# Kernel tuning notes

Hardware: AMD Instinct MI355X
Metric: run time of the kernel (lower is better)

## Reference

```python
import jax, jax.numpy as jnp
import numpy as np

L = 37       # num_landmarks
K = 8        # neighbors per landmark (uniform stand-in for ragged heatmap_dict)
HM = 512     # full heatmap size
HS = 128     # heatmap_size * scale_factor_heatmap (0.25)
HC = 64      # heatmap_size * scale_factor_cond (0.125)
DELTA = 1e-6
SP_BETA = 5.0
FFT_N = 384  # >= 255 + 128 - 1 = 382 (linear-conv safe FFT size)
BN_EPS = 1e-5


def softplus_b(x):
    # torch nn.Softplus(beta=5): log(1 + exp(beta*x)) / beta
    return jax.nn.softplus(SP_BETA * x) / SP_BETA


def resize_cubic(x, h, w):
    # stands in for F.interpolate(mode='bicubic', align_corners=False)
    return jax.image.resize(x, x.shape[:-2] + (h, w), method='cubic')


def setup_inputs() -> dict:
    key = jax.random.key(0)
    k1, k2, k3 = jax.random.split(key, 3)
    heatmaps = jax.random.normal(k1, (2, L, HM, HM), dtype=jnp.float32)
    cond_heatmaps = jax.random.normal(k2, (L, K, HC, HC), dtype=jnp.float32)
    bias = jax.random.uniform(k3, (L, K, HS, HS), dtype=jnp.float32) * 0.01
    bn_gamma = jnp.ones((L,), dtype=jnp.float32)
    bn_beta = jnp.zeros((L,), dtype=jnp.float32)
    valid_idx = jnp.asarray(
        np.stack([[(i + 1 + k) % L for k in range(K)] for i in range(L)]),
        dtype=jnp.int32)
    return {"heatmaps": heatmaps, "cond_heatmaps": cond_heatmaps, "bias": bias,
            "bn_gamma": bn_gamma, "bn_beta": bn_beta, "valid_idx": valid_idx}


def reference(heatmaps, cond_heatmaps, bias, bn_gamma, bn_beta, valid_idx):
    B = heatmaps.shape[0]
    # BatchNorm2d in training mode (batch statistics, biased variance)
    mean = jnp.mean(heatmaps, axis=(0, 2, 3))
    var = jnp.var(heatmaps, axis=(0, 2, 3))
    scale = (bn_gamma / jnp.sqrt(var + BN_EPS))[None, :, None, None]
    hm = (heatmaps - mean[None, :, None, None]) * scale + bn_beta[None, :, None, None]

    # downsample heatmaps to 128x128
    hm_rs = resize_cubic(hm, HS, HS)                      # [B, L, 128, 128]

    # priors: 64 -> 128 upsample, then softplus. [L, K, 128, 128]
    prior = softplus_b(resize_cubic(cond_heatmaps, HS, HS))

    # likelihoods: gather conditioning channels. [B, L, K, 128, 128]
    like = softplus_b(hm_rs[:, valid_idx])

    # conv_fft: pad (63, 64) each spatial side -> 255; flipped-kernel fft_conv
    # == true linear convolution, valid output 255-128+1 = 128
    pad = (HS - 1) // 2
    like_p = jnp.pad(like, ((0, 0), (0, 0), (0, 0), (pad, pad + 1), (pad, pad + 1)))
    Fb = jnp.fft.rfft2(like_p, s=(FFT_N, FFT_N))
    Fa = jnp.fft.rfft2(prior, s=(FFT_N, FFT_N))
    conv = jnp.fft.irfft2(Fb * Fa[None], s=(FFT_N, FFT_N))
    conv = conv[..., HS - 1:2 * HS - 1, HS - 1:2 * HS - 1]  # [B, L, K, 128, 128]

    # log-sum over conditioning landmarks, with learnable bias
    energy = jnp.sum(jnp.log(conv + softplus_b(bias)[None] + DELTA), axis=2)  # [B, L, 128, 128]

    # upsample x4 back to 512 and add initial (local) log-energy
    energy = resize_cubic(energy, HM, HM) + jnp.log(softplus_b(hm) + DELTA)

    # differentiable argmax2d (temperature = 1), meshgrid indexing='ij':
    # xx varies along dim -2, yy along dim -1 (as in the original code)
    soft = jax.nn.softmax(energy.reshape(B, L, -1), axis=-1).reshape(B, L, HM, HM)
    xx = jnp.arange(HM, dtype=energy.dtype)[:, None]
    yy = jnp.arange(HM, dtype=energy.dtype)[None, :]
    ex = jnp.sum(soft * xx, axis=(-2, -1))
    ey = jnp.sum(soft * yy, axis=(-2, -1))
    ones = jnp.ones_like(ex)
    return jnp.stack([ones, ex, ey], axis=-1)  # [B, L, 3]
```

## Files before the change

kernel.cpp:

```cpp
#include <hip/hip_runtime.h>
#include <hip/hip_bf16.h>
#include <math.h>

#define L_ 37
#define K_ 8
#define HM_ 512
#define HS_ 128
#define HC_ 64

using f32x4 = __attribute__((ext_vector_type(4))) float;

#define L_REGION 24656
#define PB_OFF   L_REGION
#define CONV_LDS (PB_OFF + 158*128)

static constexpr size_t OFF_SUMS   = 0;
static constexpr size_t OFF_PARAMS = 512;
static constexpr size_t OFF_TAJ    = 1024;
static constexpr size_t OFF_TAW    = 1536;
static constexpr size_t OFF_TBJ    = 9728;
static constexpr size_t OFF_TBW    = 10240;
static constexpr size_t OFF_TCJ    = 12288;
static constexpr size_t OFF_TCW    = 14336;
static constexpr size_t OFF_PART   = 22528;
static constexpr size_t OFF_TMPA   = 32768;
static constexpr size_t OFF_HMRS   = OFF_TMPA + (size_t)74*128*512*4;
static constexpr size_t OFF_PIMG   = OFF_HMRS + (size_t)74*16384*4;
static constexpr size_t OFF_EALL   = OFF_PIMG + (size_t)296*16384;
static constexpr size_t OFF_E128   = OFF_EALL + (size_t)592*16384*4;

__device__ __forceinline__ float keys_cubic(float x) {
  float out = ((1.5f * x - 2.5f) * x) * x + 1.f;
  if (x >= 1.f) out = ((-0.5f * x + 2.5f) * x - 4.f) * x + 2.f;
  if (x >= 2.f) out = 0.f;
  return out;
}
__device__ __forceinline__ float sp(float x) {
  float z = 5.f * x;
  return (fmaxf(z, 0.f) + log1pf(expf(-fabsf(z)))) * 0.2f;
}

__global__ void bn_partial_k(const float* __restrict__ heat, float* __restrict__ sums) {
  int l = blockIdx.x >> 4, seg = blockIdx.x & 15;
  int tid = threadIdx.x;
  float s = 0.f, q = 0.f;
  for (int i = tid; i < 8192; i += 256) {
    int f4 = seg * 8192 + i;
    int b = f4 >> 16, rem = f4 & 65535;
    float4 v = ((const float4*)heat)[(size_t)(b * L_ + l) * 65536 + rem];
    s += v.x + v.y + v.z + v.w;
    q += v.x*v.x + v.y*v.y + v.z*v.z + v.w*v.w;
  }
  __shared__ float rs[256], rq[256];
  rs[tid] = s; rq[tid] = q; __syncthreads();
  for (int o = 128; o > 0; o >>= 1) {
    if (tid < o) { rs[tid] += rs[tid + o]; rq[tid] += rq[tid + o]; }
    __syncthreads();
  }
  if (tid == 0) { atomicAdd(&sums[2*l], rs[0]); atomicAdd(&sums[2*l+1], rq[0]); }
}

__global__ void tables_k(int* taj, float* taw, int* tbj, float* tbw, int* tcj, float* tcw,
                         const float* __restrict__ sums, const float* __restrict__ gamma,
                         const float* __restrict__ beta, float* __restrict__ params) {
  int i = threadIdx.x;
  if (i < 128) {
    float sf = 4.f * i + 1.5f;
    int j0 = 4 * i - 6;
    taj[i] = j0;
    float w[16], sum = 0.f;
    for (int t = 0; t < 16; ++t) {
      int j = j0 + t; float ww = 0.f;
      if (j >= 0 && j < 512) ww = keys_cubic(fabsf(sf - (float)j) * 0.25f);
      w[t] = ww; sum += ww;
    }
    for (int t = 0; t < 16; ++t) taw[i*16 + t] = w[t] / sum;
    float sb = 0.5f * i - 0.25f;
    int jb = (int)floorf(sb) - 1;
    tbj[i] = jb;
    float wb[4], sumb = 0.f;
    for (int t = 0; t < 4; ++t) {
      int j = jb + t; float ww = 0.f;
      if (j >= 0 && j < 64) ww = keys_cubic(fabsf(sb - (float)j));
      wb[t] = ww; sumb += ww;
    }
    for (int t = 0; t < 4; ++t) tbw[i*4 + t] = wb[t] / sumb;
  }
  if (i < 512) {
    float sc = 0.25f * i - 0.375f;
    int jc = (int)floorf(sc) - 1;
    tcj[i] = jc;
    float wc[4], sumc = 0.f;
    for (int t = 0; t < 4; ++t) {
      int j = jc + t; float ww = 0.f;
      if (j >= 0 && j < 128) ww = keys_cubic(fabsf(sc - (float)j));
      wc[t] = ww; sumc += ww;
    }
    for (int t = 0; t < 4; ++t) tcw[i*4 + t] = wc[t] / sumc;
  }
  if (i < L_) {
    float inv = 1.f / (2.f * HM_ * HM_);
    float mean = sums[2*i] * inv;
    float var  = sums[2*i+1] * inv - mean * mean;
    float sc = gamma[i] * rsqrtf(var + 1e-5f);
    params[2*i] = sc;
    params[2*i+1] = beta[i] - mean * sc;
  }
}

__global__ void down_rows_k(const float* __restrict__ heat, const float* __restrict__ params,
                            const int* __restrict__ taj, const float* __restrict__ taw,
                            float* __restrict__ tmpA) {
  int bl = blockIdx.x >> 7;
  int i  = blockIdx.x & 127;
  int l = bl % L_;
  float sc = params[2*l], sh = params[2*l+1];
  int j0 = taj[i];
  const float* base = heat + (size_t)bl * (HM_*HM_);
  float* out = tmpA + ((size_t)bl * 128 + i) * HM_;
  float w[16];
  #pragma unroll
  for (int t = 0; t < 16; ++t) w[t] = taw[i*16 + t];
  for (int c = threadIdx.x; c < HM_; c += 256) {
    float acc = 0.f;
    #pragma unroll
    for (int t = 0; t < 16; ++t) {
      int j = min(511, max(0, j0 + t));
      acc = fmaf(w[t], fmaf(base[(size_t)j*HM_ + c], sc, sh), acc);
    }
    out[c] = acc;
  }
}

__global__ void down_cols_k(const float* __restrict__ tmpA, const int* __restrict__ taj,
                            const float* __restrict__ taw, float* __restrict__ hmrs) {
  __shared__ float row[HM_];
  int bl = blockIdx.x >> 7, i = blockIdx.x & 127;
  const float* src = tmpA + ((size_t)bl * 128 + i) * HM_;
  for (int c = threadIdx.x; c < HM_; c += 128) row[c] = src[c];
  __syncthreads();
  int ic = threadIdx.x;
  int j0 = taj[ic];
  float acc = 0.f;
  #pragma unroll
  for (int t = 0; t < 16; ++t) {
    int j = min(511, max(0, j0 + t));
    acc = fmaf(taw[ic*16 + t], row[j], acc);
  }
  hmrs[((size_t)bl * 128 + i) * 128 + ic] = acc;
}

__global__ void prior_rev_k(const float* __restrict__ cond, const int* __restrict__ tbj,
                            const float* __restrict__ tbw, unsigned char* __restrict__ pimg) {
  __shared__ float c64[HC_*HC_];
  int lk = blockIdx.x;
  const float* src = cond + (size_t)lk * HC_*HC_;
  for (int i = threadIdx.x; i < HC_*HC_; i += 256) c64[i] = src[i];
  __syncthreads();
  for (int t = threadIdx.x; t < 2048; t += 256) {
    int s = t >> 4, jblk = t & 15;
    int jy0 = tbj[s];
    float wy[4]; int jys[4];
    #pragma unroll
    for (int q = 0; q < 4; ++q) { wy[q] = tbw[s*4+q]; jys[q] = min(63, max(0, jy0 + q)); }
    float v[8];
    #pragma unroll
    for (int ii = 0; ii < 8; ++ii) {
      int j = jblk * 8 + ii;
      int jx0 = tbj[j];
      float acc = 0.f;
      #pragma unroll
      for (int q = 0; q < 4; ++q) {
        int jy = jys[q];
        float r = 0.f;
        #pragma unroll
        for (int tx = 0; tx < 4; ++tx) {
          int jx = min(63, max(0, jx0 + tx));
          r = fmaf(tbw[j*4 + tx], c64[jy*64 + jx], r);
        }
        acc = fmaf(wy[q], r, acc);
      }
      v[ii] = sp(acc);
    }
    int w0 = 0, w1 = 0;
    w0 = __builtin_amdgcn_cvt_pk_fp8_f32(v[7], v[6], w0, false);
    w0 = __builtin_amdgcn_cvt_pk_fp8_f32(v[5], v[4], w0, true);
    w1 = __builtin_amdgcn_cvt_pk_fp8_f32(v[3], v[2], w1, false);
    w1 = __builtin_amdgcn_cvt_pk_fp8_f32(v[1], v[0], w1, true);
    int cc = (15 - jblk) ^ (s & 7);
    uint2* dst = (uint2*)(pimg + (size_t)lk * 16384 + s * 128 + cc * 8);
    *dst = make_uint2((unsigned)w0, (unsigned)w1);
  }
}

__global__ __launch_bounds__(512) void conv_mfma_k(
    const float* __restrict__ hmrs, const unsigned char* __restrict__ pimg,
    const float* __restrict__ bias, const int* __restrict__ vidx,
    float* __restrict__ e_all) {
  extern __shared__ char lds[];
  int blk = blockIdx.x;
  int b = blk / 296, lk = blk % 296;
  int tid = threadIdx.x;

  {
    unsigned* lz = (unsigned*)lds;
    for (int i = tid; i < 16 + 4 + 2048; i += 512) {
      int a;
      if (i < 16) a = i;
      else if (i < 20) a = 6160 + (i - 16);
      else { int g = i - 20; int u = g >> 4, c = g & 15; a = 48*u + 48 + c; }
      lz[a] = 0u;
    }
  }
  {
    unsigned* pz = (unsigned*)(lds + PB_OFF);
    for (int i = tid; i < 960; i += 512) {
      int a = (i < 480) ? i : (18304/4 + (i - 480));
      pz[a] = 0u;
    }
  }
  int vl = vidx[lk];
  const float4* likes4 = (const float4*)(hmrs + (size_t)(b * L_ + vl) * 16384);
  for (int i = tid; i < 1024; i += 512) {
    int u = i >> 3, c16 = (i & 7) << 4;
    int base4 = u * 32 + (c16 >> 2);
    unsigned wds[4];
    #pragma unroll
    for (int q = 0; q < 4; ++q) {
      float4 v = likes4[base4 + q];
      int w = 0;
      w = __builtin_amdgcn_cvt_pk_fp8_f32(sp(v.x), sp(v.y), w, false);
      w = __builtin_amdgcn_cvt_pk_fp8_f32(sp(v.z), sp(v.w), w, true);
      wds[q] = (unsigned)w;
    }
    *(uint4*)(lds + 64 + 192*u + c16) = make_uint4(wds[0], wds[1], wds[2], wds[3]);
  }
  {
    const uint4* src = (const uint4*)(pimg + (size_t)lk * 16384);
    uint4* dst = (uint4*)(lds + PB_OFF + 15*128);
    for (int i = tid; i < 1024; i += 512) dst[i] = src[i];
  }
  __syncthreads();

  int wid = tid >> 6, lane = tid & 63;
  int wm = wid >> 2, wn = wid & 3;
  int l15 = lane & 15, kg = lane >> 4;
  int xb = wn * 32;
  int par4 = (1 + l15) & 3;
  int shiftB = par4 << 3;
  int C0 = 1 + l15 + 8*kg + xb - par4;

  f32x4 acc[4][2];
  #pragma unroll
  for (int mt = 0; mt < 4; ++mt)
    #pragma unroll
    for (int nt = 0; nt < 2; ++nt)
      #pragma unroll
      for (int j = 0; j < 4; ++j) acc[mt][nt][j] = 0.f;

  int u_lo = max(0, 64 * wm - 63);
  for (int u = u_lo; u <= 127; ++u) {
    const unsigned* bp = (const unsigned*)(lds + C0 + 192*u);
    #pragma unroll
    for (int kc = 0; kc < 4; ++kc) {
      if (xb + 95 - 32*kc < 0 || xb + 33 - 32*kc > 127) continue;
      long Bf[2];
      #pragma unroll
      for (int nt = 0; nt < 2; ++nt) {
        int q = 24 + 4*nt - 8*kc;
        unsigned d0 = bp[q], d1 = bp[q+1], d2 = bp[q+2];
        unsigned b0 = (unsigned)((((unsigned long long)d1 << 32) | d0) >> shiftB);
        unsigned b1 = (unsigned)((((unsigned long long)d2 << 32) | d1) >> shiftB);
        Bf[nt] = (long)(((unsigned long long)b1 << 32) | b0);
      }
      int cA16 = (12 - 4*kc + kg);
      #pragma unroll
      for (int mt = 0; mt < 4; ++mt) {
        int y0 = 64 * wm + 16 * mt;
        if (u < y0 - 63 || u > y0 + 79) continue;
        int rr = y0 + l15 + 79 - u;
        int swz = (cA16 ^ ((rr + 1) & 7)) << 3;
        long Af = *(const long*)(lds + PB_OFF + rr * 128 + swz);
        acc[mt][0] = __builtin_amdgcn_mfma_f32_16x16x32_fp8_fp8(Af, Bf[0], acc[mt][0], 0, 0, 0);
        acc[mt][1] = __builtin_amdgcn_mfma_f32_16x16x32_fp8_fp8(Af, Bf[1], acc[mt][1], 0, 0, 0);
      }
    }
  }

  const float* bs = bias + (size_t)lk * 16384;
  float* eo = e_all + (size_t)(b * 296 + lk) * 16384;
  int row0 = kg * 4;
  #pragma unroll
  for (int mt = 0; mt < 4; ++mt) {
    #pragma unroll
    for (int nt = 0; nt < 2; ++nt) {
      int x = xb + nt * 16 + l15;
      int yb = 64 * wm + 16 * mt + row0;
      #pragma unroll
      for (int rr = 0; rr < 4; ++rr) {
        int y = yb + rr;
        float v = acc[mt][nt][rr] + sp(bs[y * 128 + x]) + 1e-6f;
        eo[y * 128 + x] = logf(v);
      }
    }
  }
}

__global__ void esum_k(const float* __restrict__ e_all, float* __restrict__ e128) {
  int bl = blockIdx.x; int tid = threadIdx.x;
  const float4* src = (const float4*)(e_all + (size_t)bl * 8 * 16384);
  float4* dst = (float4*)(e128 + (size_t)bl * 16384);
  for (int i = tid; i < 4096; i += 256) {
    float4 a = src[i];
    #pragma unroll
    for (int k = 1; k < 8; ++k) {
      float4 v = src[k * 4096 + i];
      a.x += v.x; a.y += v.y; a.z += v.z; a.w += v.w;
    }
    dst[i] = a;
  }
}

__global__ __launch_bounds__(256) void final_partial_k(
    const float* __restrict__ heat, const float* __restrict__ params,
    const float* __restrict__ e128, const int* __restrict__ tcj, const float* __restrict__ tcw,
    float* __restrict__ partials) {
  __shared__ float Elds[20 * 128];
  __shared__ float rm[256], rS[256], ry[256], rx[256];
  int blk = blockIdx.x;
  int bl = blk >> 3, seg = blk & 7;
  int l = bl % L_;
  int tid = threadIdx.x;
  float sc = params[2*l], sh = params[2*l+1];
  int y_lo = seg * 64;
  int r_lo = max(0, tcj[y_lo]);
  int r_hi = min(127, tcj[y_lo + 63] + 3);
  int nrows = r_hi - r_lo + 1;
  const float* E = e128 + (size_t)bl * 16384;
  for (int i = tid; i < nrows * 128; i += 256) Elds[i] = E[r_lo * 128 + i];
  __syncthreads();

  float wx[2][4]; int jx[2][4];
  #pragma unroll
  for (int xi = 0; xi < 2; ++xi) {
    int x = tid + xi * 256;
    int j0 = tcj[x];
    #pragma unroll
    for (int t = 0; t < 4; ++t) { wx[xi][t] = tcw[x*4 + t]; jx[xi][t] = min(127, max(0, j0 + t)); }
  }

  float m = -1e30f, S = 0.f, Sy = 0.f, Sx = 0.f;
  for (int y = y_lo; y < y_lo + 64; ++y) {
    int jy0 = tcj[y];
    float wy[4]; int jyr[4];
    #pragma unroll
    for (int t = 0; t < 4; ++t) { wy[t] = tcw[y*4 + t]; jyr[t] = min(127, max(0, jy0 + t)) - r_lo; }
    #pragma unroll
    for (int xi = 0; xi < 2; ++xi) {
      int x = tid + xi * 256;
      float a = 0.f;
      #pragma unroll
      for (int t = 0; t < 4; ++t) {
        const float* Er = Elds + jyr[t] * 128;
        float rrow = wx[xi][0]*Er[jx[xi][0]] + wx[xi][1]*Er[jx[xi][1]]
                   + wx[xi][2]*Er[jx[xi][2]] + wx[xi][3]*Er[jx[xi][3]];
        a = fmaf(wy[t], rrow, a);
      }
      float hm = fmaf(heat[(size_t)bl * 262144 + y * 512 + x], sc, sh);
      float e = a + logf(sp(hm) + 1e-6f);
      if (e > m) {
        float f = expf(m - e);
        S *= f; Sy *= f; Sx *= f; m = e;
      }
      float w = expf(e - m);
      S += w; Sy = fmaf(w, (float)y, Sy); Sx = fmaf(w, (float)x, Sx);
    }
  }
  rm[tid] = m; rS[tid] = S; ry[tid] = Sy; rx[tid] = Sx; __syncthreads();
  for (int o = 128; o > 0; o >>= 1) {
    if (tid < o) {
      float ma = rm[tid], mb = rm[tid + o];
      float M = fmaxf(ma, mb);
      float fa = expf(ma - M), fb = expf(mb - M);
      rS[tid] = rS[tid]*fa + rS[tid+o]*fb;
      ry[tid] = ry[tid]*fa + ry[tid+o]*fb;
      rx[tid] = rx[tid]*fa + rx[tid+o]*fb;
      rm[tid] = M;
    }
    __syncthreads();
  }
  if (tid == 0) {
    float* p = partials + (size_t)blk * 4;
    p[0] = rm[0]; p[1] = rS[0]; p[2] = ry[0]; p[3] = rx[0];
  }
}

__global__ void final_combine_k(const float* __restrict__ partials, float* __restrict__ out) {
  int bl = blockIdx.x;
  if (threadIdx.x != 0) return;
  float M = -1e30f, S = 0.f, Sy = 0.f, Sx = 0.f;
  for (int i = 0; i < 8; ++i) {
    const float* p = partials + (size_t)(bl * 8 + i) * 4;
    float m2 = p[0], s2 = p[1], sy2 = p[2], sx2 = p[3];
    float Mn = fmaxf(M, m2);
    float fa = expf(M - Mn), fb = expf(m2 - Mn);
    S = S*fa + s2*fb; Sy = Sy*fa + sy2*fb; Sx = Sx*fa + sx2*fb; M = Mn;
  }
  out[bl*3 + 0] = 1.f;
  out[bl*3 + 1] = Sy / S;
  out[bl*3 + 2] = Sx / S;
}

extern "C" void kernel_launch(void* const* d_in, const int* in_sizes, int n_in,
                              void* d_out, int out_size, void* d_ws, size_t ws_size,
                              hipStream_t stream) {
  const float* heat  = (const float*)d_in[0];
  const float* cond  = (const float*)d_in[1];
  const float* bias  = (const float*)d_in[2];
  const float* gamma = (const float*)d_in[3];
  const float* beta  = (const float*)d_in[4];
  const int*   vidx  = (const int*)d_in[5];
  float* out = (float*)d_out;
  char* ws = (char*)d_ws;

  float* sums   = (float*)(ws + OFF_SUMS);
  float* params = (float*)(ws + OFF_PARAMS);
  int*   taj = (int*)(ws + OFF_TAJ);   float* taw = (float*)(ws + OFF_TAW);
  int*   tbj = (int*)(ws + OFF_TBJ);   float* tbw = (float*)(ws + OFF_TBW);
  int*   tcj = (int*)(ws + OFF_TCJ);   float* tcw = (float*)(ws + OFF_TCW);
  float* part  = (float*)(ws + OFF_PART);
  float* tmpA  = (float*)(ws + OFF_TMPA);
  float* hmrs  = (float*)(ws + OFF_HMRS);
  unsigned char* pimg = (unsigned char*)(ws + OFF_PIMG);
  float* e_all = (float*)(ws + OFF_EALL);
  float* e128  = (float*)(ws + OFF_E128);

  hipFuncSetAttribute((const void*)conv_mfma_k,
                      hipFuncAttributeMaxDynamicSharedMemorySize, CONV_LDS);

  hipMemsetAsync(sums, 0, 2 * L_ * sizeof(float), stream);
  bn_partial_k<<<L_ * 16, 256, 0, stream>>>(heat, sums);
  tables_k<<<1, 512, 0, stream>>>(taj, taw, tbj, tbw, tcj, tcw, sums, gamma, beta, params);
  down_rows_k<<<74 * 128, 256, 0, stream>>>(heat, params, taj, taw, tmpA);
  down_cols_k<<<74 * 128, 128, 0, stream>>>(tmpA, taj, taw, hmrs);
  prior_rev_k<<<L_ * K_, 256, 0, stream>>>(cond, tbj, tbw, pimg);
  conv_mfma_k<<<2 * L_ * K_, 512, CONV_LDS, stream>>>(hmrs, pimg, bias, vidx, e_all);
  esum_k<<<74, 256, 0, stream>>>(e_all, e128);
  final_partial_k<<<74 * 8, 256, 0, stream>>>(heat, params, e128, tcj, tcw, part);
  final_combine_k<<<74, 64, 0, stream>>>(part, out);
}
```

Baseline: 657.0 us.

## Fuse downsample passes, switch conv to scaled MFMA, atomically reduce energies

Measured after the change: 979.6 us. 1.49x slower.

```diff
diff --git a/kernel.cpp b/kernel.cpp
--- a/kernel.cpp
+++ b/kernel.cpp
@@ -9,10 +9,10 @@
 #define HC_ 64
 
 using f32x4 = __attribute__((ext_vector_type(4))) float;
-
-#define L_REGION 24656
-#define PB_OFF   L_REGION
-#define CONV_LDS (PB_OFF + 158*128)
+typedef int i32x8 __attribute__((ext_vector_type(8)));
+
+#define PB_OFF   32768
+#define CONV_LDS (PB_OFF + 160*128)
 
 static constexpr size_t OFF_SUMS   = 0;
 static constexpr size_t OFF_PARAMS = 512;
@@ -23,11 +23,9 @@
 static constexpr size_t OFF_TCJ    = 12288;
 static constexpr size_t OFF_TCW    = 14336;
 static constexpr size_t OFF_PART   = 22528;
-static constexpr size_t OFF_TMPA   = 32768;
-static constexpr size_t OFF_HMRS   = OFF_TMPA + (size_t)74*128*512*4;
+static constexpr size_t OFF_HMRS   = 32768;
 static constexpr size_t OFF_PIMG   = OFF_HMRS + (size_t)74*16384*4;
-static constexpr size_t OFF_EALL   = OFF_PIMG + (size_t)296*16384;
-static constexpr size_t OFF_E128   = OFF_EALL + (size_t)592*16384*4;
+static constexpr size_t OFF_E128   = OFF_PIMG + (size_t)296*16384;
 
 __device__ __forceinline__ float keys_cubic(float x) {
   float out = ((1.5f * x - 2.5f) * x) * x + 1.f;
@@ -108,46 +106,43 @@
   }
 }
 
-__global__ void down_rows_k(const float* __restrict__ heat, const float* __restrict__ params,
-                            const int* __restrict__ taj, const float* __restrict__ taw,
-                            float* __restrict__ tmpA) {
-  int bl = blockIdx.x >> 7;
-  int i  = blockIdx.x & 127;
-  int l = bl % L_;
-  float sc = params[2*l], sh = params[2*l+1];
-  int j0 = taj[i];
-  const float* base = heat + (size_t)bl * (HM_*HM_);
-  float* out = tmpA + ((size_t)bl * 128 + i) * HM_;
-  float w[16];
-  #pragma unroll
-  for (int t = 0; t < 16; ++t) w[t] = taw[i*16 + t];
-  for (int c = threadIdx.x; c < HM_; c += 256) {
-    float acc = 0.f;
+__global__ __launch_bounds__(256) void down_fused_k(
+    const float* __restrict__ heat, const int* __restrict__ taj,
+    const float* __restrict__ taw, float* __restrict__ hmrs) {
+  extern __shared__ float sds[];
+  float* in = sds;
+  float* rm = sds + 28*512;
+  int bl = blockIdx.x >> 5, ig = blockIdx.x & 31;
+  int i0 = ig * 4;
+  int j00 = 4*i0 - 6;
+  int tid = threadIdx.x;
+  const float* hb = heat + (size_t)bl * 262144;
+  for (int idx = tid; idx < 28*128; idx += 256) {
+    int jr = idx >> 7, c4 = (idx & 127) << 2;
+    int j = min(511, max(0, j00 + jr));
+    *(float4*)(in + jr*512 + c4) = *(const float4*)(hb + (size_t)j*512 + c4);
+  }
+  __syncthreads();
+  for (int idx = tid; idx < 2048; idx += 256) {
+    int ri = idx >> 9, c = idx & 511;
+    const float* wt = taw + (i0 + ri) * 16;
+    float a = 0.f;
+    #pragma unroll
+    for (int t = 0; t < 16; ++t) a = fmaf(wt[t], in[(4*ri + t)*512 + c], a);
+    rm[ri*512 + c] = a;
+  }
+  __syncthreads();
+  for (int idx = tid; idx < 512; idx += 256) {
+    int ri = idx >> 7, ic = idx & 127;
+    int j0 = taj[ic];
+    float a = 0.f;
     #pragma unroll
     for (int t = 0; t < 16; ++t) {
       int j = min(511, max(0, j0 + t));
-      acc = fmaf(w[t], fmaf(base[(size_t)j*HM_ + c], sc, sh), acc);
-    }
-    out[c] = acc;
-  }
-}
-
-__global__ void down_cols_k(const float* __restrict__ tmpA, const int* __restrict__ taj,
-                            const float* __restrict__ taw, float* __restrict__ hmrs) {
-  __shared__ float row[HM_];
-  int bl = blockIdx.x >> 7, i = blockIdx.x & 127;
-  const float* src = tmpA + ((size_t)bl * 128 + i) * HM_;
-  for (int c = threadIdx.x; c < HM_; c += 128) row[c] = src[c];
-  __syncthreads();
-  int ic = threadIdx.x;
-  int j0 = taj[ic];
-  float acc = 0.f;
-  #pragma unroll
-  for (int t = 0; t < 16; ++t) {
-    int j = min(511, max(0, j0 + t));
-    acc = fmaf(taw[ic*16 + t], row[j], acc);
-  }
-  hmrs[((size_t)bl * 128 + i) * 128 + ic] = acc;
+      a = fmaf(taw[ic*16 + t], rm[ri*512 + j], a);
+    }
+    hmrs[((size_t)bl*128 + i0 + ri)*128 + ic] = a;
+  }
 }
 
 __global__ void prior_rev_k(const float* __restrict__ cond, const int* __restrict__ tbj,
@@ -157,168 +152,156 @@
   const float* src = cond + (size_t)lk * HC_*HC_;
   for (int i = threadIdx.x; i < HC_*HC_; i += 256) c64[i] = src[i];
   __syncthreads();
-  for (int t = threadIdx.x; t < 2048; t += 256) {
-    int s = t >> 4, jblk = t & 15;
+  for (int t = threadIdx.x; t < 1024; t += 256) {
+    int s = t >> 3, c16 = t & 7;
     int jy0 = tbj[s];
     float wy[4]; int jys[4];
     #pragma unroll
     for (int q = 0; q < 4; ++q) { wy[q] = tbw[s*4+q]; jys[q] = min(63, max(0, jy0 + q)); }
-    float v[8];
-    #pragma unroll
-    for (int ii = 0; ii < 8; ++ii) {
-      int j = jblk * 8 + ii;
-      int jx0 = tbj[j];
-      float acc = 0.f;
+    unsigned w[4];
+    #pragma unroll
+    for (int q = 0; q < 4; ++q) {
+      float vv[4];
       #pragma unroll
-      for (int q = 0; q < 4; ++q) {
-        int jy = jys[q];
-        float r = 0.f;
+      for (int bq = 0; bq < 4; ++bq) {
+        int jj = 16*c16 + 4*q + bq;
+        int j = 127 - jj;
+        int jx0 = tbj[j];
+        float acc = 0.f;
         #pragma unroll
-        for (int tx = 0; tx < 4; ++tx) {
-          int jx = min(63, max(0, jx0 + tx));
-          r = fmaf(tbw[j*4 + tx], c64[jy*64 + jx], r);
+        for (int ty = 0; ty < 4; ++ty) {
+          float r = 0.f;
+          #pragma unroll
+          for (int tx = 0; tx < 4; ++tx) {
+            int jx = min(63, max(0, jx0 + tx));
+            r = fmaf(tbw[j*4 + tx], c64[jys[ty]*64 + jx], r);
+          }
+          acc = fmaf(wy[ty], r, acc);
         }
-        acc = fmaf(wy[q], r, acc);
+        vv[bq] = sp(acc);
       }
-      v[ii] = sp(acc);
-    }
-    int w0 = 0, w1 = 0;
-    w0 = __builtin_amdgcn_cvt_pk_fp8_f32(v[7], v[6], w0, false);
-    w0 = __builtin_amdgcn_cvt_pk_fp8_f32(v[5], v[4], w0, true);
-    w1 = __builtin_amdgcn_cvt_pk_fp8_f32(v[3], v[2], w1, false);
-    w1 = __builtin_amdgcn_cvt_pk_fp8_f32(v[1], v[0], w1, true);
-    int cc = (15 - jblk) ^ (s & 7);
-    uint2* dst = (uint2*)(pimg + (size_t)lk * 16384 + s * 128 + cc * 8);
-    *dst = make_uint2((unsigned)w0, (unsigned)w1);
-  }
-}
-
-__global__ __launch_bounds__(512) void conv_mfma_k(
+      int wq = 0;
+      wq = __builtin_amdgcn_cvt_pk_fp8_f32(vv[0], vv[1], wq, false);
+      wq = __builtin_amdgcn_cvt_pk_fp8_f32(vv[2], vv[3], wq, true);
+      w[q] = (unsigned)wq;
+    }
+    unsigned char* dst = pimg + (size_t)lk*16384 + s*128 + ((c16 ^ (s & 7)) << 4);
+    *(uint4*)dst = make_uint4(w[0], w[1], w[2], w[3]);
+  }
+}
+
+__global__ __launch_bounds__(256, 3) void conv_mfma_k(
     const float* __restrict__ hmrs, const unsigned char* __restrict__ pimg,
     const float* __restrict__ bias, const int* __restrict__ vidx,
-    float* __restrict__ e_all) {
+    const float* __restrict__ params, float* __restrict__ e128) {
   extern __shared__ char lds[];
+  char* Lb = lds;
+  char* Pb = lds + PB_OFF;
   int blk = blockIdx.x;
-  int b = blk / 296, lk = blk % 296;
+  int b = blk / 296, lk = blk % 296, l = lk >> 3;
   int tid = threadIdx.x;
 
   {
-    unsigned* lz = (unsigned*)lds;
-    for (int i = tid; i < 16 + 4 + 2048; i += 512) {
-      int a;
-      if (i < 16) a = i;
-      else if (i < 20) a = 6160 + (i - 16);
-      else { int g = i - 20; int u = g >> 4, c = g & 15; a = 48*u + 48 + c; }
-      lz[a] = 0u;
+    unsigned* lz = (unsigned*)Lb;
+    for (int i = tid; i < 4096; i += 256) {
+      int row = i >> 5, q = i & 31;
+      lz[row*64 + (q < 16 ? q : q + 32)] = 0u;
     }
   }
   {
-    unsigned* pz = (unsigned*)(lds + PB_OFF);
-    for (int i = tid; i < 960; i += 512) {
-      int a = (i < 480) ? i : (18304/4 + (i - 480));
-      pz[a] = 0u;
+    unsigned* pz = (unsigned*)Pb;
+    for (int i = tid; i < 1024; i += 256) {
+      int row = i >> 5;
+      pz[(row < 16 ? row : row + 128)*32 + (i & 31)] = 0u;
     }
   }
   int vl = vidx[lk];
+  float sc = params[2*vl], sh = params[2*vl + 1];
   const float4* likes4 = (const float4*)(hmrs + (size_t)(b * L_ + vl) * 16384);
-  for (int i = tid; i < 1024; i += 512) {
-    int u = i >> 3, c16 = (i & 7) << 4;
-    int base4 = u * 32 + (c16 >> 2);
+  for (int i = tid; i < 1024; i += 256) {
+    int u = i >> 3, ch = i & 7;
+    int b4 = u * 32 + ch * 4;
     unsigned wds[4];
     #pragma unroll
     for (int q = 0; q < 4; ++q) {
-      float4 v = likes4[base4 + q];
+      float4 v = likes4[b4 + q];
       int w = 0;
-      w = __builtin_amdgcn_cvt_pk_fp8_f32(sp(v.x), sp(v.y), w, false);
-      w = __builtin_amdgcn_cvt_pk_fp8_f32(sp(v.z), sp(v.w), w, true);
+      w = __builtin_amdgcn_cvt_pk_fp8_f32(sp(fmaf(v.x, sc, sh)), sp(fmaf(v.y, sc, sh)), w, false);
+      w = __builtin_amdgcn_cvt_pk_fp8_f32(sp(fmaf(v.z, sc, sh)), sp(fmaf(v.w, sc, sh)), w, true);
       wds[q] = (unsigned)w;
     }
-    *(uint4*)(lds + 64 + 192*u + c16) = make_uint4(wds[0], wds[1], wds[2], wds[3]);
+    *(uint4*)(Lb + u*256 + 64 + ch*16) = make_uint4(wds[0], wds[1], wds[2], wds[3]);
   }
   {
     const uint4* src = (const uint4*)(pimg + (size_t)lk * 16384);
-    uint4* dst = (uint4*)(lds + PB_OFF + 15*128);
-    for (int i = tid; i < 1024; i += 512) dst[i] = src[i];
+    uint4* dst = (uint4*)(Pb + 16*128);
+    for (int i = tid; i < 1024; i += 256) dst[i] = src[i];
   }
   __syncthreads();
 
   int wid = tid >> 6, lane = tid & 63;
-  int wm = wid >> 2, wn = wid & 3;
+  int wm = wid >> 1, wn = wid & 1;
   int l15 = lane & 15, kg = lane >> 4;
-  int xb = wn * 32;
-  int par4 = (1 + l15) & 3;
-  int shiftB = par4 << 3;
-  int C0 = 1 + l15 + 8*kg + xb - par4;
-
-  f32x4 acc[4][2];
+  int x0 = wn * 64, y_base = wm * 64;
+  int bb = 1 + x0 + l15 + 32*kg;
+  int bd0 = bb >> 2;
+  int shiftB = (bb & 3) * 8;
+
+  f32x4 acc[4][4];
   #pragma unroll
   for (int mt = 0; mt < 4; ++mt)
     #pragma unroll
-    for (int nt = 0; nt < 2; ++nt)
+    for (int nt = 0; nt < 4; ++nt)
       #pragma unroll
       for (int j = 0; j < 4; ++j) acc[mt][nt][j] = 0.f;
 
-  int u_lo = max(0, 64 * wm - 63);
-  for (int u = u_lo; u <= 127; ++u) {
-    const unsigned* bp = (const unsigned*)(lds + C0 + 192*u);
-    #pragma unroll
-    for (int kc = 0; kc < 4; ++kc) {
-      if (xb + 95 - 32*kc < 0 || xb + 33 - 32*kc > 127) continue;
-      long Bf[2];
+  int u_lo = wm ? 1 : 0;
+  #pragma unroll 1
+  for (int u = u_lo; u < 128; ++u) {
+    const unsigned* Lr = (const unsigned*)(Lb + (u << 8));
+    unsigned d[21];
+    #pragma unroll
+    for (int q = 0; q < 21; ++q) d[q] = Lr[bd0 + q];
+    i32x8 Bf[4];
+    #pragma unroll
+    for (int nt = 0; nt < 4; ++nt)
       #pragma unroll
-      for (int nt = 0; nt < 2; ++nt) {
-        int q = 24 + 4*nt - 8*kc;
-        unsigned d0 = bp[q], d1 = bp[q+1], d2 = bp[q+2];
-        unsigned b0 = (unsigned)((((unsigned long long)d1 << 32) | d0) >> shiftB);
-        unsigned b1 = (unsigned)((((unsigned long long)d2 << 32) | d1) >> shiftB);
-        Bf[nt] = (long)(((unsigned long long)b1 << 32) | b0);
+      for (int j = 0; j < 8; ++j)
+        Bf[nt][j] = (int)(unsigned)((((unsigned long long)d[4*nt + j + 1] << 32) | d[4*nt + j]) >> shiftB);
+    #pragma unroll
+    for (int mt = 0; mt < 4; ++mt) {
+      int yt = y_base + 16*mt;
+      if (u < yt - 63 || u > yt + 79) continue;
+      int r = yt + l15 + 80 - u;
+      const char* pr = Pb + (r << 7);
+      int m8 = r & 7;
+      uint4 alo = *(const uint4*)(pr + (((2*kg)     ^ m8) << 4));
+      uint4 ahi = *(const uint4*)(pr + (((2*kg + 1) ^ m8) << 4));
+      i32x8 Af;
+      Af[0] = (int)alo.x; Af[1] = (int)alo.y; Af[2] = (int)alo.z; Af[3] = (int)alo.w;
+      Af[4] = (int)ahi.x; Af[5] = (int)ahi.y; Af[6] = (int)ahi.z; Af[7] = (int)ahi.w;
+      #pragma unroll
+      for (int nt = 0; nt < 4; ++nt)
+        acc[mt][nt] = __builtin_amdgcn_mfma_scale_f32_16x16x128_f8f6f4(
+            Af, Bf[nt], acc[mt][nt], 0, 0, 0, 0x7F7F7F7F, 0, 0x7F7F7F7F);
+    }
+  }
+
+  const float* bs = bias + (size_t)lk * 16384;
+  float* e = e128 + (size_t)(b * L_ + l) * 16384;
+  #pragma unroll
+  for (int mt = 0; mt < 4; ++mt)
+    #pragma unroll
+    for (int nt = 0; nt < 4; ++nt) {
+      int x = x0 + nt*16 + l15;
+      int yb = y_base + mt*16 + kg*4;
+      #pragma unroll
+      for (int rg = 0; rg < 4; ++rg) {
+        int y = yb + rg;
+        float v = acc[mt][nt][rg] + sp(bs[y*128 + x]) + 1e-6f;
+        atomicAdd(&e[y*128 + x], logf(v));
       }
-      int cA16 = (12 - 4*kc + kg);
-      #pragma unroll
-      for (int mt = 0; mt < 4; ++mt) {
-        int y0 = 64 * wm + 16 * mt;
-        if (u < y0 - 63 || u > y0 + 79) continue;
-        int rr = y0 + l15 + 79 - u;
-        int swz = (cA16 ^ ((rr + 1) & 7)) << 3;
-        long Af = *(const long*)(lds + PB_OFF + rr * 128 + swz);
-        acc[mt][0] = __builtin_amdgcn_mfma_f32_16x16x32_fp8_fp8(Af, Bf[0], acc[mt][0], 0, 0, 0);
-        acc[mt][1] = __builtin_amdgcn_mfma_f32_16x16x32_fp8_fp8(Af, Bf[1], acc[mt][1], 0, 0, 0);
-      }
-    }
-  }
-
-  const float* bs = bias + (size_t)lk * 16384;
-  float* eo = e_all + (size_t)(b * 296 + lk) * 16384;
-  int row0 = kg * 4;
-  #pragma unroll
-  for (int mt = 0; mt < 4; ++mt) {
-    #pragma unroll
-    for (int nt = 0; nt < 2; ++nt) {
-      int x = xb + nt * 16 + l15;
-      int yb = 64 * wm + 16 * mt + row0;
-      #pragma unroll
-      for (int rr = 0; rr < 4; ++rr) {
-        int y = yb + rr;
-        float v = acc[mt][nt][rr] + sp(bs[y * 128 + x]) + 1e-6f;
-        eo[y * 128 + x] = logf(v);
-      }
-    }
-  }
-}
-
-__global__ void esum_k(const float* __restrict__ e_all, float* __restrict__ e128) {
-  int bl = blockIdx.x; int tid = threadIdx.x;
-  const float4* src = (const float4*)(e_all + (size_t)bl * 8 * 16384);
-  float4* dst = (float4*)(e128 + (size_t)bl * 16384);
-  for (int i = tid; i < 4096; i += 256) {
-    float4 a = src[i];
-    #pragma unroll
-    for (int k = 1; k < 8; ++k) {
-      float4 v = src[k * 4096 + i];
-      a.x += v.x; a.y += v.y; a.z += v.z; a.w += v.w;
-    }
-    dst[i] = a;
-  }
+    }
 }
 
 __global__ __launch_bounds__(256) void final_partial_k(
@@ -326,6 +309,7 @@
     const float* __restrict__ e128, const int* __restrict__ tcj, const float* __restrict__ tcw,
     float* __restrict__ partials) {
   __shared__ float Elds[20 * 128];
+  __shared__ float Eh[20 * 512];
   __shared__ float rm[256], rS[256], ry[256], rx[256];
   int blk = blockIdx.x;
   int bl = blk >> 3, seg = blk & 7;
@@ -339,15 +323,18 @@
   const float* E = e128 + (size_t)bl * 16384;
   for (int i = tid; i < nrows * 128; i += 256) Elds[i] = E[r_lo * 128 + i];
   __syncthreads();
-
-  float wx[2][4]; int jx[2][4];
-  #pragma unroll
-  for (int xi = 0; xi < 2; ++xi) {
-    int x = tid + xi * 256;
+  for (int idx = tid; idx < (nrows << 9); idx += 256) {
+    int r = idx >> 9, x = idx & 511;
     int j0 = tcj[x];
-    #pragma unroll
-    for (int t = 0; t < 4; ++t) { wx[xi][t] = tcw[x*4 + t]; jx[xi][t] = min(127, max(0, j0 + t)); }
-  }
+    float a = 0.f;
+    #pragma unroll
+    for (int t = 0; t < 4; ++t) {
+      int j = min(127, max(0, j0 + t));
+      a = fmaf(tcw[x*4 + t], Elds[r*128 + j], a);
+    }
+    Eh[r*512 + x] = a;
+  }
+  __syncthreads();
 
   float m = -1e30f, S = 0.f, Sy = 0.f, Sx = 0.f;
   for (int y = y_lo; y < y_lo + 64; ++y) {
@@ -358,14 +345,8 @@
     #pragma unroll
     for (int xi = 0; xi < 2; ++xi) {
       int x = tid + xi * 256;
-      float a = 0.f;
-      #pragma unroll
-      for (int t = 0; t < 4; ++t) {
-        const float* Er = Elds + jyr[t] * 128;
-        float rrow = wx[xi][0]*Er[jx[xi][0]] + wx[xi][1]*Er[jx[xi][1]]
-                   + wx[xi][2]*Er[jx[xi][2]] + wx[xi][3]*Er[jx[xi][3]];
-        a = fmaf(wy[t], rrow, a);
-      }
+      float a = wy[0]*Eh[jyr[0]*512 + x] + wy[1]*Eh[jyr[1]*512 + x]
+              + wy[2]*Eh[jyr[2]*512 + x] + wy[3]*Eh[jyr[3]*512 + x];
       float hm = fmaf(heat[(size_t)bl * 262144 + y * 512 + x], sc, sh);
       float e = a + logf(sp(hm) + 1e-6f);
       if (e > m) {
@@ -429,23 +410,23 @@
   int*   tbj = (int*)(ws + OFF_TBJ);   float* tbw = (float*)(ws + OFF_TBW);
   int*   tcj = (int*)(ws + OFF_TCJ);   float* tcw = (float*)(ws + OFF_TCW);
   float* part  = (float*)(ws + OFF_PART);
-  float* tmpA  = (float*)(ws + OFF_TMPA);
   float* hmrs  = (float*)(ws + OFF_HMRS);
   unsigned char* pimg = (unsigned char*)(ws + OFF_PIMG);
-  float* e_all = (float*)(ws + OFF_EALL);
   float* e128  = (float*)(ws + OFF_E128);
 
   hipFuncSetAttribute((const void*)conv_mfma_k,
                       hipFuncAttributeMaxDynamicSharedMemorySize, CONV_LDS);
+  hipFuncSetAttribute((const void*)down_fused_k,
+                      hipFuncAttributeMaxDynamicSharedMemorySize, 32*512*4);
 
   hipMemsetAsync(sums, 0, 2 * L_ * sizeof(float), stream);
+  hipMemsetAsync(e128, 0, (size_t)74 * 16384 * 4, stream);
+
   bn_partial_k<<<L_ * 16, 256, 0, stream>>>(heat, sums);
   tables_k<<<1, 512, 0, stream>>>(taj, taw, tbj, tbw, tcj, tcw, sums, gamma, beta, params);
-  down_rows_k<<<74 * 128, 256, 0, stream>>>(heat, params, taj, taw, tmpA);
-  down_cols_k<<<74 * 128, 128, 0, stream>>>(tmpA, taj, taw, hmrs);
+  down_fused_k<<<74 * 32, 256, 32*512*4, stream>>>(heat, taj, taw, hmrs);
   prior_rev_k<<<L_ * K_, 256, 0, stream>>>(cond, tbj, tbw, pimg);
-  conv_mfma_k<<<2 * L_ * K_, 512, CONV_LDS, stream>>>(hmrs, pimg, bias, vidx, e_all);
-  esum_k<<<74, 256, 0, stream>>>(e_all, e128);
+  conv_mfma_k<<<2 * L_ * K_, 256, CONV_LDS, stream>>>(hmrs, pimg, bias, vidx, params, e128);
   final_partial_k<<<74 * 8, 256, 0, stream>>>(heat, params, e128, tcj, tcw, part);
   final_combine_k<<<74, 64, 0, stream>>>(part, out);
 }
```
